# Kernel tuning notes

Hardware: AMD Instinct MI355X
Metric: run time of the kernel (lower is better)

The kernel has to match this reference:

```python
import jax, jax.numpy as jnp
import numpy as np

N_CLASSES = 10


def setup_inputs() -> dict:
    key = jax.random.key(0)
    k1, k2, k3 = jax.random.split(key, 3)
    x_test = jax.random.uniform(k1, (2048, 784), dtype=jnp.float32)
    x_train = jax.random.uniform(k2, (50000, 784), dtype=jnp.float32)
    y_train = jax.random.randint(k3, (50000,), 0, N_CLASSES, dtype=jnp.int64)
    return {"x_test": x_test, "x_train": x_train, "y_train": y_train, "k": 5}


def reference(x_test, x_train, y_train, k):
    B = x_test.shape[0]
    xt = x_test.reshape(B, -1)                      # [B, D]
    xdb = x_train.reshape(x_train.shape[0], -1)     # [N, D]
    # similarity: matches on 1s + matches on 0s (binary-pixel Hamming-like score)
    dist_full = xt @ xdb.T + (1.0 - xt) @ (1.0 - xdb).T   # [B, N]
    _, idx = jax.lax.top_k(dist_full, k)            # [B, k] nearest-neighbor indices
    yk = y_train[idx]                               # [B, k] neighbor labels
    # per-row mode vote; argmax over class-count histogram == torch's
    counts = jnp.sum(jax.nn.one_hot(yk, N_CLASSES, dtype=jnp.int32), axis=1)  # [B, C]
    return jnp.argmax(counts, axis=1)
```

## Files before the change

kernel.cpp:

```cpp
#include <hip/hip_runtime.h>
#include <float.h>
#include <stdint.h>

#define D_DIM 784
#define KPADB 896
#define N_TRAIN 50000
#define NPAD 50048
#define B_TEST 2048
#define N_CLASSES 10
#define TOPK 5
#define NBLK 391
#define SEL 8
#define SBIAS 12645136

typedef __attribute__((ext_vector_type(4))) int int4v;

__device__ inline unsigned umax32(unsigned a, unsigned b) { return a > b ? a : b; }

__device__ inline void ins8(unsigned long long* tk, unsigned long long v) {
    #pragma unroll
    for (int s = 0; s < SEL; ++s) {
        unsigned long long mx = v > tk[s] ? v : tk[s];
        unsigned long long mn = v > tk[s] ? tk[s] : v;
        tk[s] = mx; v = mn;
    }
}

__device__ inline void ins5u(unsigned* tk, unsigned v) {
    #pragma unroll
    for (int s = 0; s < TOPK; ++s) {
        unsigned mx = v > tk[s] ? v : tk[s];
        unsigned mn = v > tk[s] ? tk[s] : v;
        tk[s] = mx; v = mn;
    }
}

#define INSERT5(tvarr, tiarr, CV, CI)                                   \
    {                                                                   \
        float _cv = (CV); int _ci = (CI);                               \
        _Pragma("unroll")                                               \
        for (int _s = 0; _s < TOPK; ++_s) {                             \
            bool _bet = (_cv > tvarr[_s]) ||                            \
                        (_cv == tvarr[_s] && _ci < tiarr[_s]);          \
            float _fv = _bet ? tvarr[_s] : _cv;                         \
            int   _fi = _bet ? tiarr[_s] : _ci;                         \
            tvarr[_s] = _bet ? _cv : tvarr[_s];                         \
            tiarr[_s] = _bet ? _ci : tiarr[_s];                         \
            _cv = _fv; _ci = _fi;                                       \
        }                                                               \
    }

__device__ inline unsigned pack4q(float4 f) {
    int q0 = __float2int_rn(fmaf(f.x, 254.f, -127.f));
    int q1 = __float2int_rn(fmaf(f.y, 254.f, -127.f));
    int q2 = __float2int_rn(fmaf(f.z, 254.f, -127.f));
    int q3 = __float2int_rn(fmaf(f.w, 254.f, -127.f));
    return (unsigned)(q0 & 255) | ((unsigned)(q1 & 255) << 8) |
           ((unsigned)(q2 & 255) << 16) | ((unsigned)(q3 & 255) << 24);
}

__global__ __launch_bounds__(256)
void quant_kernel(const float* __restrict__ xtr, const float* __restrict__ xte,
                  char* __restrict__ Bq, char* __restrict__ Aq) {
    const int blk = blockIdx.x;
    const float* src;
    char* dst;
    int rows_src, row;
    if (blk < NPAD / 4) {
        src = xtr; dst = Bq; rows_src = N_TRAIN;
        row = blk * 4 + (threadIdx.x >> 6);
    } else {
        src = xte; dst = Aq; rows_src = B_TEST;
        row = (blk - NPAD / 4) * 4 + (threadIdx.x >> 6);
        if (row >= B_TEST) return;
    }
    const int lane = threadIdx.x & 63;
    if (lane >= 56) return;
    uint4 w = {0u, 0u, 0u, 0u};
    if (row < rows_src && lane < 49) {
        const float4* p = (const float4*)(src + (size_t)row * D_DIM + lane * 16);
        w.x = pack4q(p[0]);
        w.y = pack4q(p[1]);
        w.z = pack4q(p[2]);
        w.w = pack4q(p[3]);
    }
    *(uint4*)(dst + (size_t)row * KPADB + lane * 16) = w;
}

__global__ __launch_bounds__(256, 4)
void knn_mfma(const char* __restrict__ Aq, const char* __restrict__ Bq,
              unsigned* __restrict__ cval) {
    const int bid = blockIdx.x;
    const int xcd = bid & 7;
    const int sidx = bid >> 3;
    const int st_g = (sidx >> 4) * 8 + xcd;
    const int r16 = sidx & 15;
    const int mblk = (st_g & 3) * 4 + (r16 & 3);
    const int nchunk = (st_g >> 2) * 4 + (r16 >> 2);
    if (nchunk >= NBLK) return;

    __shared__ char lds_raw[39936] __attribute__((aligned(16)));
    unsigned* epi  = (unsigned*)lds_raw;
    unsigned* lval = (unsigned*)(lds_raw + 34816);

    const int tid = threadIdx.x;
    const int w = tid >> 6, lane = tid & 63;
    const int l15 = lane & 15, q = lane >> 4;
    const int mb = mblk * 128, nb = nchunk * 128;
    const int mw = (w & 1) * 64, nw = (w >> 1) * 64;

    const int s_tile = w >> 1, s_half = w & 1;
    const char* sbase = (s_tile == 0) ? (Aq + (size_t)mb * KPADB)
                                      : (Bq + (size_t)nb * KPADB);
    const char* srow = sbase + (size_t)s_half * 64 * KPADB;
    char* ldsw = lds_raw + s_tile * 16384 + s_half * 8192;

    int choff[8];
    #pragma unroll
    for (int c = 0; c < 8; ++c) {
        int s = c * 64 + lane;
        int rl = s >> 3;
        int k8 = (s & 7) ^ (rl & 7);
        choff[c] = rl * KPADB + k8 * 16;
    }
    int aoff[4][2], boff[4][2];
    #pragma unroll
    for (int k64 = 0; k64 < 2; ++k64) {
        int ch = ((k64 * 4 + q) ^ (l15 & 7)) * 16;
        #pragma unroll
        for (int i = 0; i < 4; ++i) {
            aoff[i][k64] = (mw + i * 16 + l15) * 128 + ch;
            boff[i][k64] = (nw + i * 16 + l15) * 128 + ch;
        }
    }

    int4v acc[4][4];
    #pragma unroll
    for (int i = 0; i < 4; ++i)
        #pragma unroll
        for (int j = 0; j < 4; ++j)
            acc[i][j] = (int4v){0, 0, 0, 0};

    for (int kt = 0; kt < KPADB; kt += 128) {
        #pragma unroll
        for (int c = 0; c < 8; ++c) {
            __builtin_amdgcn_global_load_lds(
                (const __attribute__((address_space(1))) void*)(srow + choff[c] + kt),
                (__attribute__((address_space(3))) void*)(ldsw + c * 1024),
                16, 0, 0);
        }
        __syncthreads();
        #pragma unroll
        for (int k64 = 0; k64 < 2; ++k64) {
            int4v a[4], b[4];
            #pragma unroll
            for (int i = 0; i < 4; ++i) a[i] = *(const int4v*)(lds_raw + aoff[i][k64]);
            #pragma unroll
            for (int j = 0; j < 4; ++j) b[j] = *(const int4v*)(lds_raw + 16384 + boff[j][k64]);
            #pragma unroll
            for (int i = 0; i < 4; ++i)
                #pragma unroll
                for (int j = 0; j < 4; ++j)
                    acc[i][j] = __builtin_amdgcn_mfma_i32_16x16x64_i8(a[i], b[j], acc[i][j], 0, 0, 0);
        }
        __syncthreads();
    }

    int okn[4];
    #pragma unroll
    for (int j = 0; j < 4; ++j) okn[j] = (nb + nw + j * 16 + l15 < N_TRAIN);

    for (int h = 0; h < 2; ++h) {
        __syncthreads();
        if ((w & 1) == h) {
            #pragma unroll
            for (int i = 0; i < 4; ++i) {
                int r = i * 16 + q * 4;
                #pragma unroll
                for (int j = 0; j < 4; ++j) {
                    int col = nw + j * 16 + l15;
                    uint4 kv;
                    if (okn[j]) {
                        int4v s = acc[i][j];
                        kv.x = ((unsigned)(s.x + SBIAS) << 7) | (unsigned)col;
                        kv.y = ((unsigned)(s.y + SBIAS) << 7) | (unsigned)col;
                        kv.z = ((unsigned)(s.z + SBIAS) << 7) | (unsigned)col;
                        kv.w = ((unsigned)(s.w + SBIAS) << 7) | (unsigned)col;
                    } else {
                        kv.x = kv.y = kv.z = kv.w = (unsigned)col;
                    }
                    *(uint4*)(epi + col * 68 + r) = kv;
                }
            }
        }
        __syncthreads();
        {
            int r = tid & 63, qq = tid >> 6;
            const unsigned* ebase = epi + (qq * 32) * 68 + r;
            unsigned tv5[TOPK] = {0u, 0u, 0u, 0u, 0u};
            #pragma unroll
            for (int c = 0; c < 32; ++c) ins5u(tv5, ebase[c * 68]);
            #pragma unroll
            for (int s = 0; s < TOPK; ++s) lval[(r * 4 + qq) * TOPK + s] = tv5[s];
        }
        __syncthreads();
        if (tid < 64) {
            unsigned tv[TOPK] = {0u, 0u, 0u, 0u, 0u};
            for (int qq = 0; qq < 4; ++qq)
                #pragma unroll
                for (int s = 0; s < TOPK; ++s) {
                    unsigned cv = lval[(tid * 4 + qq) * TOPK + s];
                    if (cv > tv[TOPK - 1]) ins5u(tv, cv);
                }
            int grow = mb + h * 64 + tid;
            size_t base = ((size_t)grow * NBLK + nchunk) * TOPK;
            #pragma unroll
            for (int s = 0; s < TOPK; ++s) cval[base + s] = tv[s];
        }
    }
}

__global__ __launch_bounds__(256)
void knn_final(const unsigned* __restrict__ cval,
               const float* __restrict__ xt, const float* __restrict__ xtr,
               const int* __restrict__ y, int* __restrict__ out) {
    __shared__ unsigned long long sv[256][SEL];
    __shared__ double cs[SEL];
    __shared__ int    cn[SEL];
    const int b = blockIdx.x;
    const int t = threadIdx.x;

    unsigned long long tk[SEL];
    #pragma unroll
    for (int s = 0; s < SEL; ++s) tk[s] = 0ull;

    const unsigned* row = cval + (size_t)b * (NBLK * TOPK);
    for (int e = t; e < NBLK * TOPK; e += 256) {
        unsigned v = row[e];
        int chunk = e / TOPK;
        unsigned n = (unsigned)chunk * 128u + (v & 127u);
        unsigned long long v64 = ((unsigned long long)v << 16) | n;
        if (v64 > tk[SEL - 1]) ins8(tk, v64);
    }
    #pragma unroll
    for (int s = 0; s < SEL; ++s) sv[t][s] = tk[s];
    __syncthreads();

    for (int off = 128; off >= 1; off >>= 1) {
        if (t < off) {
            if (sv[t + off][0] > tk[SEL - 1]) {
                #pragma unroll
                for (int s = 0; s < SEL; ++s) {
                    unsigned long long v = sv[t + off][s];
                    if (v > tk[SEL - 1]) ins8(tk, v);
                }
                #pragma unroll
                for (int s = 0; s < SEL; ++s) sv[t][s] = tk[s];
            }
        }
        __syncthreads();
    }

    const int w = t >> 6, lane = t & 63, half = lane >> 5, hl = lane & 31;
    const int c = w * 2 + half;
    {
        int n = (int)(sv[0][c] & 0xFFFFull);
        double dot = 0.0, rs = 0.0;
        if (n < N_TRAIN) {
            const float4* pa = (const float4*)(xt + (size_t)b * D_DIM);
            const float4* pb = (const float4*)(xtr + (size_t)n * D_DIM);
            #pragma unroll
            for (int jj = 0; jj < 7; ++jj) {
                int j = hl + jj * 32;
                if (j < 196) {
                    float4 a = pa[j], bb = pb[j];
                    dot += (double)a.x * bb.x + (double)a.y * bb.y +
                           (double)a.z * bb.z + (double)a.w * bb.w;
                    rs  += (double)bb.x + (double)bb.y + (double)bb.z + (double)bb.w;
                }
            }
        }
        #pragma unroll
        for (int off = 16; off > 0; off >>= 1) {
            dot += __shfl_down(dot, off, 32);
            rs  += __shfl_down(rs, off, 32);
        }
        if (hl == 0) {
            cs[c] = (n < N_TRAIN) ? (2.0 * dot - rs) : -1.0e300;
            cn[c] = n;
        }
    }
    __syncthreads();

    if (t == 0) {
        double bv[TOPK]; int bi[TOPK];
        #pragma unroll
        for (int s = 0; s < TOPK; ++s) { bv[s] = -1.0e300; bi[s] = 0x7fffffff; }
        for (int cc = 0; cc < SEL; ++cc) {
            double cv = cs[cc]; int ci = cn[cc];
            #pragma unroll
            for (int s = 0; s < TOPK; ++s) {
                bool bet = (cv > bv[s]) || (cv == bv[s] && ci < bi[s]);
                double fv = bet ? bv[s] : cv;
                int    fi = bet ? bi[s] : ci;
                bv[s] = bet ? cv : bv[s];
                bi[s] = bet ? ci : bi[s];
                cv = fv; ci = fi;
            }
        }
        int lab[TOPK];
        #pragma unroll
        for (int s = 0; s < TOPK; ++s) lab[s] = y[bi[s]];
        int best_c = 0, best_cnt = -1;
        #pragma unroll
        for (int cc = 0; cc < N_CLASSES; ++cc) {
            int cnt = 0;
            #pragma unroll
            for (int s = 0; s < TOPK; ++s) cnt += (lab[s] == cc) ? 1 : 0;
            if (cnt > best_cnt) { best_cnt = cnt; best_c = cc; }
        }
        out[b] = best_c;
    }
}

#define FBM 64
#define FBN 64
#define FBK 16
#define FNCH 32
#define FCHUNK 1600

__global__ __launch_bounds__(256)
void rowsum_kernel(const float* __restrict__ x, float* __restrict__ s) {
    int row = blockIdx.x * 4 + (threadIdx.x >> 6);
    int lane = threadIdx.x & 63;
    if (row >= N_TRAIN) return;
    const float* p = x + (size_t)row * D_DIM;
    float acc = 0.f;
    for (int i = lane; i < D_DIM; i += 64) acc += p[i];
    #pragma unroll
    for (int off = 32; off > 0; off >>= 1) acc += __shfl_down(acc, off, 64);
    if (lane == 0) s[row] = acc;
}

__global__ __launch_bounds__(256)
void knn_phaseA_fb(const float* __restrict__ xt, const float* __restrict__ xtr,
                   const float* __restrict__ strain,
                   float* __restrict__ cval, int* __restrict__ cidx) {
    __shared__ float As[FBK][FBM + 4];
    __shared__ float Bs[FBK][FBN + 4];
    __shared__ float lv[FBM][16][TOPK];
    __shared__ int   li[FBM][16][TOPK];

    const int tid = threadIdx.x;
    const int tx = tid & 15, ty = tid >> 4;
    const int b0 = blockIdx.x * FBM;
    const int chunk = blockIdx.y;
    const int n_base = chunk * FCHUNK;
    const int lrow = tid >> 2;
    const int lk4  = (tid & 3) * 4;

    float tv[4][TOPK]; int ti[4][TOPK];
    #pragma unroll
    for (int i = 0; i < 4; ++i)
        #pragma unroll
        for (int s = 0; s < TOPK; ++s) { tv[i][s] = -FLT_MAX; ti[i][s] = 0x7fffffff; }

    for (int nt = 0; nt < FCHUNK; nt += FBN) {
        const int n0 = n_base + nt;
        double accd[4][4];
        #pragma unroll
        for (int i = 0; i < 4; ++i)
            #pragma unroll
            for (int j = 0; j < 4; ++j) accd[i][j] = 0.0;

        for (int kt = 0; kt < D_DIM; kt += FBK) {
            float4 av = *(const float4*)(xt + (size_t)(b0 + lrow) * D_DIM + kt + lk4);
            As[lk4 + 0][lrow] = av.x; As[lk4 + 1][lrow] = av.y;
            As[lk4 + 2][lrow] = av.z; As[lk4 + 3][lrow] = av.w;
            int nr = n0 + lrow;
            float4 bv = make_float4(0.f, 0.f, 0.f, 0.f);
            if (nr < N_TRAIN) bv = *(const float4*)(xtr + (size_t)nr * D_DIM + kt + lk4);
            Bs[lk4 + 0][lrow] = bv.x; Bs[lk4 + 1][lrow] = bv.y;
            Bs[lk4 + 2][lrow] = bv.z; Bs[lk4 + 3][lrow] = bv.w;
            __syncthreads();

            float accf[4][4] = {{0.f}};
            #pragma unroll
            for (int k = 0; k < FBK; ++k) {
                float a[4], b[4];
                #pragma unroll
                for (int i = 0; i < 4; ++i) a[i] = As[k][ty * 4 + i];
                #pragma unroll
                for (int j = 0; j < 4; ++j) b[j] = Bs[k][tx * 4 + j];
                #pragma unroll
                for (int i = 0; i < 4; ++i)
                    #pragma unroll
                    for (int j = 0; j < 4; ++j) accf[i][j] += a[i] * b[j];
            }
            #pragma unroll
            for (int i = 0; i < 4; ++i)
                #pragma unroll
                for (int j = 0; j < 4; ++j) accd[i][j] += (double)accf[i][j];
            __syncthreads();
        }

        #pragma unroll
        for (int j = 0; j < 4; ++j) {
            int n = n0 + tx * 4 + j;
            if (n < N_TRAIN) {
                float sn = strain[n];
                #pragma unroll
                for (int i = 0; i < 4; ++i) {
                    float sc = (float)(2.0 * accd[i][j] - (double)sn);
                    if (sc > tv[i][TOPK - 1] ||
                        (sc == tv[i][TOPK - 1] && n < ti[i][TOPK - 1])) {
                        INSERT5(tv[i], ti[i], sc, n);
                    }
                }
            }
        }
    }

    #pragma unroll
    for (int i = 0; i < 4; ++i)
        #pragma unroll
        for (int s = 0; s < TOPK; ++s) {
            lv[ty * 4 + i][tx][s] = tv[i][s];
            li[ty * 4 + i][tx][s] = ti[i][s];
        }
    __syncthreads();

    if (tid < FBM) {
        float bv5[TOPK]; int bi5[TOPK];
        #pragma unroll
        for (int s = 0; s < TOPK; ++s) { bv5[s] = -FLT_MAX; bi5[s] = 0x7fffffff; }
        for (int tt = 0; tt < 16; ++tt)
            #pragma unroll
            for (int s = 0; s < TOPK; ++s) {
                float cv = lv[tid][tt][s]; int ci = li[tid][tt][s];
                if (cv > bv5[TOPK - 1] || (cv == bv5[TOPK - 1] && ci < bi5[TOPK - 1])) {
                    INSERT5(bv5, bi5, cv, ci);
                }
            }
        size_t base = ((size_t)(b0 + tid) * FNCH + chunk) * TOPK;
        #pragma unroll
        for (int s = 0; s < TOPK; ++s) { cval[base + s] = bv5[s]; cidx[base + s] = bi5[s]; }
    }
}

__global__ __launch_bounds__(256)
void knn_phaseB_fb(const float* __restrict__ cval, const int* __restrict__ cidx,
                   const int* __restrict__ y, int* __restrict__ out) {
    int b = blockIdx.x * blockDim.x + threadIdx.x;
    if (b >= B_TEST) return;
    const float* v = cval + (size_t)b * FNCH * TOPK;
    const int* ix = cidx + (size_t)b * FNCH * TOPK;
    float bv5[TOPK]; int bi5[TOPK];
    #pragma unroll
    for (int s = 0; s < TOPK; ++s) { bv5[s] = -FLT_MAX; bi5[s] = 0x7fffffff; }
    for (int tt = 0; tt < FNCH * TOPK; ++tt) {
        float cv = v[tt]; int ci = ix[tt];
        if (cv > bv5[TOPK - 1] || (cv == bv5[TOPK - 1] && ci < bi5[TOPK - 1])) {
            INSERT5(bv5, bi5, cv, ci);
        }
    }
    int lab[TOPK];
    #pragma unroll
    for (int s = 0; s < TOPK; ++s) lab[s] = y[bi5[s]];
    int best_c = 0, best_cnt = -1;
    #pragma unroll
    for (int cc = 0; cc < N_CLASSES; ++cc) {
        int cnt = 0;
        #pragma unroll
        for (int s = 0; s < TOPK; ++s) cnt += (lab[s] == cc) ? 1 : 0;
        if (cnt > best_cnt) { best_cnt = cnt; best_c = cc; }
    }
    out[b] = best_c;
}

extern "C" void kernel_launch(void* const* d_in, const int* in_sizes, int n_in,
                              void* d_out, int out_size, void* d_ws, size_t ws_size,
                              hipStream_t stream) {
    const float* x_test  = (const float*)d_in[0];
    const float* x_train = (const float*)d_in[1];
    const int*   y_train = (const int*)d_in[2];
    int* out = (int*)d_out;

    const size_t sz_Bq  = (size_t)NPAD * KPADB;
    const size_t off_Aq = sz_Bq;
    const size_t sz_Aq  = (size_t)B_TEST * KPADB;
    const size_t off_cv = off_Aq + sz_Aq;
    const size_t sz_cv  = (size_t)B_TEST * NBLK * TOPK * 4;
    const size_t need   = off_cv + sz_cv;

    char* ws = (char*)d_ws;

    if (ws_size >= need) {
        char* Bq = ws;
        char* Aq = ws + off_Aq;
        unsigned* cval = (unsigned*)(ws + off_cv);

        quant_kernel<<<NPAD / 4 + B_TEST / 4, 256, 0, stream>>>(
            x_train, x_test, Bq, Aq);

        knn_mfma<<<6272, 256, 0, stream>>>(Aq, Bq, cval);

        knn_final<<<B_TEST, 256, 0, stream>>>(cval, x_test, x_train, y_train, out);
    } else {
        float* strain = (float*)ws;
        rowsum_kernel<<<N_TRAIN / 4, 256, 0, stream>>>(x_train, strain);
        float* cval = (float*)(ws + 200192);
        int*   cidx = (int*)(ws + 200192 + (size_t)B_TEST * FNCH * TOPK * 4);

        dim3 gridA(B_TEST / FBM, FNCH);
        knn_phaseA_fb<<<gridA, 256, 0, stream>>>(x_test, x_train, strain, cval, cidx);
        knn_phaseB_fb<<<(B_TEST + 255) / 256, 256, 0, stream>>>(cval, cidx, y_train, out);
    }
}
```

Baseline: 384.3 us.

## Double-buffer int8 MFMA K-loop with 64-wide tiles and trim K padding

Splits the int8 GEMM K loop into 13 tiles of 64 bytes instead of 7 tiles of 128. Each iteration issues the async global-to-LDS copy of the next tile into a second LDS buffer before computing the current one, so one barrier per tile replaces two and loads overlap the MFMAs. The K padding drops from 896 to 832, which removes the zero-padded MFMA work and reduces quantized bytes written and read. The LDS swizzle and offsets are rewritten for 64-byte rows; a wrong swizzle would cause bank conflicts or wrong results.

After: 390.3 us. Within noise of the previous version (+1.6%).

```diff
diff --git a/kernel.cpp b/kernel.cpp
--- a/kernel.cpp
+++ b/kernel.cpp
@@ -3,7 +3,7 @@
 #include <stdint.h>
 
 #define D_DIM 784
-#define KPADB 896
+#define KPADB 832
 #define N_TRAIN 50000
 #define NPAD 50048
 #define B_TEST 2048
@@ -12,6 +12,7 @@
 #define NBLK 391
 #define SEL 8
 #define SBIAS 12645136
+#define NT 13
 
 typedef __attribute__((ext_vector_type(4))) int int4v;
 
@@ -75,7 +76,7 @@
         if (row >= B_TEST) return;
     }
     const int lane = threadIdx.x & 63;
-    if (lane >= 56) return;
+    if (lane >= 52) return;
     uint4 w = {0u, 0u, 0u, 0u};
     if (row < rows_src && lane < 49) {
         const float4* p = (const float4*)(src + (size_t)row * D_DIM + lane * 16);
@@ -113,25 +114,22 @@
     const char* sbase = (s_tile == 0) ? (Aq + (size_t)mb * KPADB)
                                       : (Bq + (size_t)nb * KPADB);
     const char* srow = sbase + (size_t)s_half * 64 * KPADB;
-    char* ldsw = lds_raw + s_tile * 16384 + s_half * 8192;
-
-    int choff[8];
-    #pragma unroll
-    for (int c = 0; c < 8; ++c) {
+    const int ldsw_off = s_tile * 8192 + s_half * 4096;
+
+    int choff[4];
+    #pragma unroll
+    for (int c = 0; c < 4; ++c) {
         int s = c * 64 + lane;
-        int rl = s >> 3;
-        int k8 = (s & 7) ^ (rl & 7);
-        choff[c] = rl * KPADB + k8 * 16;
-    }
-    int aoff[4][2], boff[4][2];
-    #pragma unroll
-    for (int k64 = 0; k64 < 2; ++k64) {
-        int ch = ((k64 * 4 + q) ^ (l15 & 7)) * 16;
-        #pragma unroll
-        for (int i = 0; i < 4; ++i) {
-            aoff[i][k64] = (mw + i * 16 + l15) * 128 + ch;
-            boff[i][k64] = (nw + i * 16 + l15) * 128 + ch;
-        }
+        int rl = s >> 2;
+        int k4 = (s & 3) ^ ((rl >> 1) & 3);
+        choff[c] = rl * KPADB + k4 * 16;
+    }
+    const int ch = (q ^ ((l15 >> 1) & 3)) * 16;
+    int aoff[4], boff[4];
+    #pragma unroll
+    for (int i = 0; i < 4; ++i) {
+        aoff[i] = (mw + i * 16 + l15) * 64 + ch;
+        boff[i] = (nw + i * 16 + l15) * 64 + ch;
     }
 
     int4v acc[4][4];
@@ -141,30 +139,45 @@
         for (int j = 0; j < 4; ++j)
             acc[i][j] = (int4v){0, 0, 0, 0};
 
-    for (int kt = 0; kt < KPADB; kt += 128) {
-        #pragma unroll
-        for (int c = 0; c < 8; ++c) {
-            __builtin_amdgcn_global_load_lds(
-                (const __attribute__((address_space(1))) void*)(srow + choff[c] + kt),
-                (__attribute__((address_space(3))) void*)(ldsw + c * 1024),
-                16, 0, 0);
-        }
+    #define STAGE_TILE(BUF, KT)                                               \
+        {                                                                     \
+            char* dst_ = lds_raw + (BUF) * 16384 + ldsw_off;                  \
+            _Pragma("unroll")                                                 \
+            for (int c_ = 0; c_ < 4; ++c_) {                                  \
+                __builtin_amdgcn_global_load_lds(                             \
+                    (const __attribute__((address_space(1))) void*)           \
+                        (srow + choff[c_] + (KT)),                            \
+                    (__attribute__((address_space(3))) void*)(dst_ + c_ * 1024),\
+                    16, 0, 0);                                                \
+            }                                                                 \
+        }
+
+    #define COMPUTE_TILE(BUF)                                                 \
+        {                                                                     \
+            const char* ab_ = lds_raw + (BUF) * 16384;                        \
+            int4v a_[4], b_[4];                                               \
+            _Pragma("unroll")                                                 \
+            for (int i_ = 0; i_ < 4; ++i_) a_[i_] = *(const int4v*)(ab_ + aoff[i_]); \
+            _Pragma("unroll")                                                 \
+            for (int j_ = 0; j_ < 4; ++j_) b_[j_] = *(const int4v*)(ab_ + 8192 + boff[j_]); \
+            _Pragma("unroll")                                                 \
+            for (int i_ = 0; i_ < 4; ++i_)                                    \
+                _Pragma("unroll")                                             \
+                for (int j_ = 0; j_ < 4; ++j_)                                \
+                    acc[i_][j_] = __builtin_amdgcn_mfma_i32_16x16x64_i8(      \
+                        a_[i_], b_[j_], acc[i_][j_], 0, 0, 0);                \
+        }
+
+    STAGE_TILE(0, 0);
+    __syncthreads();
+    for (int t = 0; t < NT - 1; ++t) {
+        const int cur = t & 1;
+        STAGE_TILE(cur ^ 1, (t + 1) * 64);
+        __builtin_amdgcn_sched_barrier(0);
+        COMPUTE_TILE(cur);
         __syncthreads();
-        #pragma unroll
-        for (int k64 = 0; k64 < 2; ++k64) {
-            int4v a[4], b[4];
-            #pragma unroll
-            for (int i = 0; i < 4; ++i) a[i] = *(const int4v*)(lds_raw + aoff[i][k64]);
-            #pragma unroll
-            for (int j = 0; j < 4; ++j) b[j] = *(const int4v*)(lds_raw + 16384 + boff[j][k64]);
-            #pragma unroll
-            for (int i = 0; i < 4; ++i)
-                #pragma unroll
-                for (int j = 0; j < 4; ++j)
-                    acc[i][j] = __builtin_amdgcn_mfma_i32_16x16x64_i8(a[i], b[j], acc[i][j], 0, 0, 0);
-        }
-        __syncthreads();
-    }
+    }
+    COMPUTE_TILE(0);
 
     int okn[4];
     #pragma unroll
@@ -218,6 +231,8 @@
             for (int s = 0; s < TOPK; ++s) cval[base + s] = tv[s];
         }
     }
+    #undef STAGE_TILE
+    #undef COMPUTE_TILE
 }
 
 __global__ __launch_bounds__(256)
```
